# Performance work log

Hardware: AMD Instinct MI355X
Metric: run time of the kernel (lower is better)

## Reference

```python
import jax, jax.numpy as jnp
import numpy as np

HEADS = 8
DIM_HEAD = 64
SCALE = 10.0
EPS = 1e-12  # F.normalize eps


def setup_inputs() -> dict:
    key = jax.random.key(0)
    k1, k2, k3, k4 = jax.random.split(key, 4)
    dim, hidden = 256, HEADS * DIM_HEAD
    x = jax.random.normal(k1, (8, dim, 32, 32), dtype=jnp.float32)
    w_qkv = jax.random.normal(k2, (3 * hidden, dim), dtype=jnp.float32) * (1.0 / np.sqrt(dim))
    w_out = jax.random.normal(k3, (dim, hidden), dtype=jnp.float32) * (1.0 / np.sqrt(hidden))
    b_out = jax.random.normal(k4, (dim,), dtype=jnp.float32) * 0.01
    return {"x": x, "w_qkv": w_qkv, "w_out": w_out, "b_out": b_out}


def _l2norm_last(t):
    # matches F.normalize(t, dim=-1): t / max(||t||_2, eps)
    n = jnp.sqrt(jnp.sum(t * t, axis=-1, keepdims=True))
    return t / jnp.maximum(n, EPS)


def reference(x, w_qkv, w_out, b_out):
    b, c, hh, ww = x.shape
    n = hh * ww
    # 1x1 conv == channel matmul
    qkv = jnp.einsum('bcxy,oc->boxy', x, w_qkv)  # (b, 3*hidden, h, w)
    q, k, v = jnp.split(qkv, 3, axis=1)
    # 'b (h c) x y -> b h c (x y)'
    to_heads = lambda t: t.reshape(b, HEADS, DIM_HEAD, n)
    q, k, v = to_heads(q), to_heads(k), to_heads(v)
    # NOTE: l2norm over the LAST axis = spatial token axis n (faithful to source)
    q = _l2norm_last(q)
    k = _l2norm_last(k)
    sim = jnp.einsum('bhdi,bhdj->bhij', q, k) * SCALE  # (b, h, n, n)
    attn = jax.nn.softmax(sim, axis=-1)
    out = jnp.einsum('bhij,bhdj->bhid', attn, v)  # (b, h, n, d)
    # 'b h (x y) d -> b (h d) x y'
    out = out.transpose(0, 1, 3, 2).reshape(b, HEADS * DIM_HEAD, hh, ww)
    return jnp.einsum('bcxy,oc->boxy', out, w_out) + b_out[None, :, None, None]
```

## Files before the change

### kernel.cpp

```cpp
#include <hip/hip_runtime.h>
#include <math.h>

#define NHEADS 8
#define DHEAD  64
#define HIDDEN 512
#define CIN    256
#define NTOK   1024
#define QK_SCALE 10.0f
#define LOG2E 1.44269504088896f
#define MSHIFT 10.5f
#define MBIAS  (-MSHIFT * LOG2E)

typedef __bf16 bf16x8 __attribute__((ext_vector_type(8)));
typedef float  f32x4  __attribute__((ext_vector_type(4)));
typedef unsigned u32x4 __attribute__((ext_vector_type(4)));
typedef unsigned short u16x8 __attribute__((ext_vector_type(8)));
typedef unsigned short u16x4 __attribute__((ext_vector_type(4)));

__device__ inline unsigned short f2bf(float f) {
    unsigned u = __builtin_bit_cast(unsigned, f);
    u = (u + 0x7FFFu + ((u >> 16) & 1u)) >> 16;
    return (unsigned short)u;
}

__device__ inline unsigned pk2(float a, float b) {
    return (unsigned)f2bf(a) | ((unsigned)f2bf(b) << 16);
}

__device__ inline float bf2f(unsigned short u) {
    return __builtin_bit_cast(float, (unsigned)u << 16);
}

__device__ inline bf16x8 cvt8(const float* p) {
    float4 a = *(const float4*)p;
    float4 b = *(const float4*)(p + 4);
    u16x8 t;
    t[0] = f2bf(a.x); t[1] = f2bf(a.y); t[2] = f2bf(a.z); t[3] = f2bf(a.w);
    t[4] = f2bf(b.x); t[5] = f2bf(b.y); t[6] = f2bf(b.z); t[7] = f2bf(b.w);
    return __builtin_bit_cast(bf16x8, t);
}

__global__ __launch_bounds__(256)
void cvt_x_kernel(const float* __restrict__ x, unsigned short* __restrict__ xt) {
    const int b  = blockIdx.z;
    const int c0 = blockIdx.y * 64;
    const int n0 = blockIdx.x * 64;
    const float* src = x + ((size_t)b * CIN + c0) * NTOK + n0;
    unsigned short* dst = xt + ((size_t)b * NTOK + n0) * CIN + c0;

    __shared__ float T[64][65];
    const int t = threadIdx.x;
    {
        const int nq = t & 15, cg = t >> 4;
        #pragma unroll
        for (int rr = 0; rr < 4; ++rr) {
            const int c = cg + rr * 16;
            float4 v = *(const float4*)(src + (size_t)c * NTOK + nq * 4);
            T[c][nq * 4 + 0] = v.x;
            T[c][nq * 4 + 1] = v.y;
            T[c][nq * 4 + 2] = v.z;
            T[c][nq * 4 + 3] = v.w;
        }
    }
    __syncthreads();
    {
        const int n = t >> 2, cq = t & 3;
        alignas(16) unsigned short tmp[16];
        #pragma unroll
        for (int e = 0; e < 16; ++e)
            tmp[e] = f2bf(T[cq * 16 + e][n]);
        *(uint4*)(dst + (size_t)n * CIN + cq * 16)     = *(uint4*)&tmp[0];
        *(uint4*)(dst + (size_t)n * CIN + cq * 16 + 8) = *(uint4*)&tmp[8];
    }
}

__global__ __launch_bounds__(256)
void cvt_w_kernel(const float* __restrict__ wq, const float* __restrict__ wo,
                  unsigned short* __restrict__ wqb, unsigned short* __restrict__ wob) {
    const size_t i = ((size_t)blockIdx.x * 256 + threadIdx.x) * 8;
    if (i < (size_t)1536 * 256) {
        *(bf16x8*)(wqb + i) = cvt8(wq + i);
    } else {
        const size_t j = i - (size_t)1536 * 256;
        *(bf16x8*)(wob + j) = cvt8(wo + j);
    }
}

__global__ __launch_bounds__(256)
void gemm1_kernel(const unsigned short* __restrict__ wqb,
                  const unsigned short* __restrict__ xt,
                  float* __restrict__ qt,
                  unsigned short* __restrict__ vb,
                  float* __restrict__ ss) {
    const int b  = blockIdx.z;
    const int bm = blockIdx.y * 128;
    const int bn = blockIdx.x * 128;
    const int wave = threadIdx.x >> 6, lane = threadIdx.x & 63;
    const int lo = lane & 15, hi = lane >> 4;
    const int wm = bm + (wave >> 1) * 64;
    const int wn = bn + (wave & 1) * 64;

    const unsigned short* Ab = wqb + (size_t)(wm + lo) * CIN + hi * 8;
    const unsigned short* Bb = xt + ((size_t)b * NTOK + wn + lo) * CIN + hi * 8;

    f32x4 acc[4][4];
    #pragma unroll
    for (int mi = 0; mi < 4; ++mi)
        #pragma unroll
        for (int ni = 0; ni < 4; ++ni) acc[mi][ni] = (f32x4){0.f, 0.f, 0.f, 0.f};

    for (int k0 = 0; k0 < CIN; k0 += 32) {
        bf16x8 a[4], bf[4];
        #pragma unroll
        for (int mi = 0; mi < 4; ++mi) a[mi]  = *(const bf16x8*)(Ab + (size_t)mi * 16 * CIN + k0);
        #pragma unroll
        for (int ni = 0; ni < 4; ++ni) bf[ni] = *(const bf16x8*)(Bb + (size_t)ni * 16 * CIN + k0);
        #pragma unroll
        for (int mi = 0; mi < 4; ++mi)
            #pragma unroll
            for (int ni = 0; ni < 4; ++ni)
                acc[mi][ni] = __builtin_amdgcn_mfma_f32_16x16x32_bf16(a[mi], bf[ni], acc[mi][ni], 0, 0, 0);
    }

    __shared__ unsigned short VL[4][32][72];

    if (bm < 1024) {
        const int isK = (wm >= 512) ? 1 : 0;
        const int ch0 = wm & 511;
        const int head = ch0 >> 6;
        float* dst = qt + (((size_t)isK * 64 + b * 8 + head) * NTOK) * DHEAD;
        #pragma unroll
        for (int mi = 0; mi < 4; ++mi) {
            const int d = mi * 16 + hi * 4;
            #pragma unroll
            for (int ni = 0; ni < 4; ++ni) {
                const int n = wn + ni * 16 + lo;
                *(f32x4*)(dst + (size_t)n * DHEAD + d) = acc[mi][ni];
            }
        }
        float p[4][4];
        #pragma unroll
        for (int mi = 0; mi < 4; ++mi)
            #pragma unroll
            for (int r = 0; r < 4; ++r) {
                float s = 0.f;
                #pragma unroll
                for (int ni = 0; ni < 4; ++ni) s += acc[mi][ni][r] * acc[mi][ni][r];
                p[mi][r] = s;
            }
        #pragma unroll
        for (int off = 1; off < 16; off <<= 1)
            #pragma unroll
            for (int mi = 0; mi < 4; ++mi)
                #pragma unroll
                for (int r = 0; r < 4; ++r)
                    p[mi][r] += __shfl_xor(p[mi][r], off, 64);
        if (lo == 0) {
            #pragma unroll
            for (int mi = 0; mi < 4; ++mi)
                #pragma unroll
                for (int r = 0; r < 4; ++r)
                    atomicAdd(&ss[(size_t)b * 1024 + isK * 512 + ch0 + mi * 16 + hi * 4 + r], p[mi][r]);
        }
    } else {
        const int ch0 = wm - 1024;
        #pragma unroll
        for (int half = 0; half < 2; ++half) {
            #pragma unroll
            for (int mm = 0; mm < 2; ++mm) {
                const int mi = half * 2 + mm;
                #pragma unroll
                for (int ni = 0; ni < 4; ++ni)
                    #pragma unroll
                    for (int r = 0; r < 4; ++r)
                        VL[wave][mm * 16 + hi * 4 + r][ni * 16 + lo] = f2bf(acc[mi][ni][r]);
            }
            #pragma unroll
            for (int i = 0; i < 4; ++i) {
                const int flat = i * 64 + lane;
                const int row = flat >> 3, c = flat & 7;
                const int tb = c >> 2, hg = c & 3;
                const uint2 vlo = *(uint2*)&VL[wave][row][tb * 32 + hg * 4];
                const uint2 vhi = *(uint2*)&VL[wave][row][tb * 32 + hg * 4 + 16];
                uint4 v = make_uint4(vlo.x, vlo.y, vhi.x, vhi.y);
                const int ch = ch0 + half * 32 + row;
                *(uint4*)(vb + ((size_t)b * HIDDEN + ch) * NTOK + wn + c * 8) = v;
            }
        }
    }
}

__global__ __launch_bounds__(256)
void scale_cvt_kernel(const float* __restrict__ qt, const float* __restrict__ ss,
                      unsigned short* __restrict__ qs, unsigned short* __restrict__ ks) {
    const size_t idx = ((size_t)blockIdx.x * 256 + threadIdx.x) * 8;
    const size_t half = (size_t)64 * NTOK * DHEAD;
    const int isK = idx >= half;
    const size_t rem = idx - (size_t)isK * half;
    const int bh = (int)(rem >> 16);
    const int d0 = (int)(rem & 63);
    const int b  = bh >> 3;
    const int ch = isK * 512 + (bh & 7) * 64 + d0;
    const float scl = isK ? 1.0f : QK_SCALE;

    const float* ip = qt + idx;
    float4 v0 = *(const float4*)ip;
    float4 v1 = *(const float4*)(ip + 4);
    float4 q0 = *(const float4*)(ss + (size_t)b * 1024 + ch);
    float4 q1 = *(const float4*)(ss + (size_t)b * 1024 + ch + 4);
    float4 s0, s1;
    s0.x = 1.0f / fmaxf(sqrtf(q0.x), 1e-12f); s0.y = 1.0f / fmaxf(sqrtf(q0.y), 1e-12f);
    s0.z = 1.0f / fmaxf(sqrtf(q0.z), 1e-12f); s0.w = 1.0f / fmaxf(sqrtf(q0.w), 1e-12f);
    s1.x = 1.0f / fmaxf(sqrtf(q1.x), 1e-12f); s1.y = 1.0f / fmaxf(sqrtf(q1.y), 1e-12f);
    s1.z = 1.0f / fmaxf(sqrtf(q1.z), 1e-12f); s1.w = 1.0f / fmaxf(sqrtf(q1.w), 1e-12f);
    u16x8 t;
    t[0] = f2bf(v0.x * s0.x * scl); t[1] = f2bf(v0.y * s0.y * scl);
    t[2] = f2bf(v0.z * s0.z * scl); t[3] = f2bf(v0.w * s0.w * scl);
    t[4] = f2bf(v1.x * s1.x * scl); t[5] = f2bf(v1.y * s1.y * scl);
    t[6] = f2bf(v1.z * s1.z * scl); t[7] = f2bf(v1.w * s1.w * scl);
    *(u16x8*)((isK ? ks : qs) + rem) = t;
}

__global__ __launch_bounds__(128)
void attn_mfma_kernel(const unsigned short* __restrict__ qs,
                      const unsigned short* __restrict__ ks,
                      const unsigned short* __restrict__ vb,
                      unsigned short* __restrict__ po, float* __restrict__ pml) {
    const int hw = blockIdx.x;
    const int virt = (hw & 7) * 256 + (hw >> 3);
    const int bh  = virt >> 5;
    const int sub = virt & 31;
    const int it  = sub & 15;
    const int js  = sub >> 4;
    const int b = bh >> 3, h = bh & 7;

    const int lane = threadIdx.x & 63;
    const int wave = threadIdx.x >> 6;
    const int lo = lane & 15;
    const int hi = lane >> 4;
    const int iw = it * 64 + wave * 32;

    const unsigned short* qbh = qs + (size_t)bh * NTOK * DHEAD;
    const unsigned short* kbh = ks + (size_t)bh * NTOK * DHEAD;
    const unsigned short* vbh = vb + ((size_t)b * HIDDEN + h * DHEAD) * NTOK;

    bf16x8 aQ[2][2];
    #pragma unroll
    for (int f = 0; f < 2; ++f) {
        const unsigned short* qp = qbh + (size_t)(iw + f * 16 + lo) * DHEAD + hi * 8;
        aQ[f][0] = *(const bf16x8*)qp;
        aQ[f][1] = *(const bf16x8*)(qp + 32);
    }

    float lsum4[2][4];
    #pragma unroll
    for (int f = 0; f < 2; ++f)
        #pragma unroll
        for (int r = 0; r < 4; ++r) lsum4[f][r] = 0.0f;
    f32x4 acc[2][4];
    #pragma unroll
    for (int f = 0; f < 2; ++f)
        #pragma unroll
        for (int ds = 0; ds < 4; ++ds) acc[f][ds] = (f32x4){0.f, 0.f, 0.f, 0.f};

    for (int jt = 0; jt < 8; ++jt) {
        const int j0 = js * 512 + jt * 64;

        bf16x8 bV[4][2];
        #pragma unroll
        for (int ds = 0; ds < 4; ++ds) {
            const unsigned short* vp = vbh + (size_t)(ds * 16 + lo) * NTOK + j0 + hi * 8;
            bV[ds][0] = *(const bf16x8*)vp;
            bV[ds][1] = *(const bf16x8*)(vp + 32);
        }

        bf16x8 bK[4][2];
        #pragma unroll
        for (int jj = 0; jj < 4; ++jj) {
            const unsigned short* kp = kbh + (size_t)(j0 + jj * 16 + lo) * DHEAD + hi * 8;
            bK[jj][0] = *(const bf16x8*)kp;
            bK[jj][1] = *(const bf16x8*)(kp + 32);
        }

        f32x4 s[2][4];
        __builtin_amdgcn_s_setprio(1);
        #pragma unroll
        for (int jj = 0; jj < 4; ++jj)
            #pragma unroll
            for (int f = 0; f < 2; ++f) {
                f32x4 c = (f32x4){0.f, 0.f, 0.f, 0.f};
                c = __builtin_amdgcn_mfma_f32_16x16x32_bf16(bK[jj][0], aQ[f][0], c, 0, 0, 0);
                c = __builtin_amdgcn_mfma_f32_16x16x32_bf16(bK[jj][1], aQ[f][1], c, 0, 0, 0);
                s[f][jj] = c;
            }
        __builtin_amdgcn_s_setprio(0);

        unsigned pw[2][2][4];
        #pragma unroll
        for (int f = 0; f < 2; ++f) {
            #pragma unroll
            for (int jj = 0; jj < 4; ++jj)
                #pragma unroll
                for (int r = 0; r < 4; ++r) {
                    const float p = __builtin_amdgcn_exp2f(fmaf(s[f][jj][r], LOG2E, MBIAS));
                    s[f][jj][r] = p;
                    lsum4[f][r] += p;
                }
            #pragma unroll
            for (int t = 0; t < 2; ++t) {
                pw[f][t][0] = pk2(s[f][2 * t][0],     s[f][2 * t][1]);
                pw[f][t][1] = pk2(s[f][2 * t][2],     s[f][2 * t][3]);
                pw[f][t][2] = pk2(s[f][2 * t + 1][0], s[f][2 * t + 1][1]);
                pw[f][t][3] = pk2(s[f][2 * t + 1][2], s[f][2 * t + 1][3]);
            }
        }

        __builtin_amdgcn_s_setprio(1);
        #pragma unroll
        for (int ds = 0; ds < 4; ++ds)
            #pragma unroll
            for (int f = 0; f < 2; ++f)
                #pragma unroll
                for (int t = 0; t < 2; ++t) {
                    const bf16x8 bp = __builtin_bit_cast(bf16x8,
                        (u32x4){pw[f][t][0], pw[f][t][1], pw[f][t][2], pw[f][t][3]});
                    acc[f][ds] = __builtin_amdgcn_mfma_f32_16x16x32_bf16(bV[ds][t], bp, acc[f][ds], 0, 0, 0);
                }
        __builtin_amdgcn_s_setprio(0);
    }

    float lsum[2];
    #pragma unroll
    for (int f = 0; f < 2; ++f) {
        lsum[f] = (lsum4[f][0] + lsum4[f][1]) + (lsum4[f][2] + lsum4[f][3]);
        lsum[f] += __shfl_xor(lsum[f], 16, 64);
        lsum[f] += __shfl_xor(lsum[f], 32, 64);
    }

    unsigned short* pob = po + ((size_t)(js * 64 + bh) * NTOK + iw) * DHEAD;
    #pragma unroll
    for (int f = 0; f < 2; ++f) {
        #pragma unroll
        for (int ds = 0; ds < 4; ++ds) {
            uint2 w;
            w.x = pk2(acc[f][ds][0], acc[f][ds][1]);
            w.y = pk2(acc[f][ds][2], acc[f][ds][3]);
            *(uint2*)(pob + (size_t)(f * 16 + lo) * DHEAD + ds * 16 + hi * 4) = w;
        }
        if (hi == 0)
            pml[(size_t)(js * 64 + bh) * NTOK + iw + f * 16 + lo] = lsum[f];
    }
}

__global__ __launch_bounds__(256)
void combine_kernel(const unsigned short* __restrict__ po, const float* __restrict__ pml,
                    unsigned short* __restrict__ attn_t) {
    const size_t fl = ((size_t)blockIdx.x * 256 + threadIdx.x) * 4;
    const int bh  = (int)(fl >> 16);
    const int rem = (int)(fl & 65535);
    const int row = rem >> 6;
    const int d   = rem & 63;
    const int b = bh >> 3, h = bh & 7;
    const size_t SS = (size_t)64 * NTOK * DHEAD;

    const float l1 = pml[(size_t)bh * NTOK + row];
    const float l2 = pml[(size_t)(64 + bh) * NTOK + row];
    const float inv = 1.0f / (l1 + l2);

    const u16x4 o1 = *(const u16x4*)(po + fl);
    const u16x4 o2 = *(const u16x4*)(po + SS + fl);
    u16x4 r;
    #pragma unroll
    for (int e = 0; e < 4; ++e)
        r[e] = f2bf((bf2f(o1[e]) + bf2f(o2[e])) * inv);
    *(u16x4*)(attn_t + ((size_t)b * NTOK + row) * HIDDEN + h * DHEAD + d) = r;
}

__global__ __launch_bounds__(128)
void gemm2_kernel(const unsigned short* __restrict__ wob,
                  const unsigned short* __restrict__ attn_t,
                  const float* __restrict__ b_out,
                  float* __restrict__ out) {
    const int b  = blockIdx.z;
    const int bm = blockIdx.y * 64;
    const int bn = blockIdx.x * 128;
    const int wave = threadIdx.x >> 6, lane = threadIdx.x & 63;
    const int lo = lane & 15, hi = lane >> 4;
    const int wn = bn + wave * 64;

    const unsigned short* Ab = wob + (size_t)(bm + lo) * HIDDEN + hi * 8;
    const unsigned short* Bb = attn_t + ((size_t)b * NTOK + wn + lo) * HIDDEN + hi * 8;

    f32x4 acc[4][4];
    #pragma unroll
    for (int mi = 0; mi < 4; ++mi)
        #pragma unroll
        for (int ni = 0; ni < 4; ++ni) acc[mi][ni] = (f32x4){0.f, 0.f, 0.f, 0.f};

    for (int k0 = 0; k0 < HIDDEN; k0 += 32) {
        bf16x8 a[4], bf[4];
        #pragma unroll
        for (int mi = 0; mi < 4; ++mi) a[mi]  = *(const bf16x8*)(Ab + (size_t)mi * 16 * HIDDEN + k0);
        #pragma unroll
        for (int ni = 0; ni < 4; ++ni) bf[ni] = *(const bf16x8*)(Bb + (size_t)ni * 16 * HIDDEN + k0);
        #pragma unroll
        for (int mi = 0; mi < 4; ++mi)
            #pragma unroll
            for (int ni = 0; ni < 4; ++ni)
                acc[mi][ni] = __builtin_amdgcn_mfma_f32_16x16x32_bf16(a[mi], bf[ni], acc[mi][ni], 0, 0, 0);
    }

    __shared__ float OL[2][32][69];
    #pragma unroll
    for (int half = 0; half < 2; ++half) {
        #pragma unroll
        for (int mm = 0; mm < 2; ++mm) {
            const int mi = half * 2 + mm;
            #pragma unroll
            for (int ni = 0; ni < 4; ++ni)
                #pragma unroll
                for (int r = 0; r < 4; ++r)
                    OL[wave][mm * 16 + hi * 4 + r][ni * 16 + lo] = acc[mi][ni][r];
        }
        #pragma unroll
        for (int i = 0; i < 8; ++i) {
            const int flat = i * 64 + lane;
            const int row = flat >> 4, c = flat & 15;
            float4 v = *(float4*)&OL[wave][row][c * 4];
            const int m = bm + half * 32 + row;
            const float bb = b_out[m];
            v.x += bb; v.y += bb; v.z += bb; v.w += bb;
            *(float4*)(out + ((size_t)b * CIN + m) * NTOK + wn + c * 4) = v;
        }
    }
}

extern "C" void kernel_launch(void* const* d_in, const int* in_sizes, int n_in,
                              void* d_out, int out_size, void* d_ws, size_t ws_size,
                              hipStream_t stream) {
    const float* x     = (const float*)d_in[0];
    const float* w_qkv = (const float*)d_in[1];
    const float* w_out = (const float*)d_in[2];
    const float* b_out = (const float*)d_in[3];
    float* out = (float*)d_out;

    char* ws = (char*)d_ws;
    unsigned short* xt  = (unsigned short*)(ws);
    unsigned short* wqb = (unsigned short*)(ws + 4194304);
    unsigned short* wob = (unsigned short*)(ws + 4980736);
    float*          ss  = (float*)(ws + 5242880);
    unsigned short* qs  = (unsigned short*)(ws + 5308416);
    unsigned short* ks  = (unsigned short*)(ws + 13697024);
    unsigned short* vb  = (unsigned short*)(ws + 22085632);
    float*          qt  = (float*)(ws + 30474240);
    unsigned short* po  = (unsigned short*)(ws + 30474240);
    unsigned short* attn_t = (unsigned short*)(ws + 5308416);
    float*          pml = (float*)(ws + 64028672);

    hipMemsetAsync(ss, 0, 8 * 1024 * sizeof(float), stream);

    cvt_x_kernel<<<dim3(16, 4, 8), 256, 0, stream>>>(x, xt);
    cvt_w_kernel<<<256, 256, 0, stream>>>(w_qkv, w_out, wqb, wob);

    gemm1_kernel<<<dim3(8, 12, 8), 256, 0, stream>>>(wqb, xt, qt, vb, ss);

    scale_cvt_kernel<<<4096, 256, 0, stream>>>(qt, ss, qs, ks);

    attn_mfma_kernel<<<2048, 128, 0, stream>>>(qs, ks, vb, po, pml);

    combine_kernel<<<4096, 256, 0, stream>>>(po, pml, attn_t);

    gemm2_kernel<<<dim3(8, 4, 8), 128, 0, stream>>>(wob, attn_t, b_out, out);
}
```

Before: 203.5 us.

## Split attention keys four ways and pack probabilities by bf16 truncation

The attention kernel now splits each query tile's keys across four partitions instead of two. This doubles the block count to 4096, halves the per-block loop, and unrolls it by two, aiming at better occupancy and latency hiding. Probability packing switches from round-to-nearest to bit truncation, and the row sums accumulate the truncated values so numerator and denominator stay consistent. The combine kernel sums four partials and processes eight elements per thread, but now reads twice as much partial-output data from memory, and the larger po/pml buffers depend on the workspace being big enough.

```diff
diff --git a/kernel.cpp b/kernel.cpp
--- a/kernel.cpp
+++ b/kernel.cpp
@@ -10,6 +10,7 @@
 #define LOG2E 1.44269504088896f
 #define MSHIFT 10.5f
 #define MBIAS  (-MSHIFT * LOG2E)
+#define NSPLIT 4
 
 typedef __bf16 bf16x8 __attribute__((ext_vector_type(8)));
 typedef float  f32x4  __attribute__((ext_vector_type(4)));
@@ -25,6 +26,14 @@
 
 __device__ inline unsigned pk2(float a, float b) {
     return (unsigned)f2bf(a) | ((unsigned)f2bf(b) << 16);
+}
+
+__device__ inline unsigned pk2t(float a, float b) {
+    return (__builtin_bit_cast(unsigned, a) >> 16) |
+           (__builtin_bit_cast(unsigned, b) & 0xFFFF0000u);
+}
+__device__ inline float trunc_bf(float f) {
+    return __builtin_bit_cast(float, __builtin_bit_cast(unsigned, f) & 0xFFFF0000u);
 }
 
 __device__ inline float bf2f(unsigned short u) {
@@ -227,9 +236,9 @@
                       const unsigned short* __restrict__ vb,
                       unsigned short* __restrict__ po, float* __restrict__ pml) {
     const int hw = blockIdx.x;
-    const int virt = (hw & 7) * 256 + (hw >> 3);
-    const int bh  = virt >> 5;
-    const int sub = virt & 31;
+    const int virt = (hw & 7) * 512 + (hw >> 3);
+    const int bh  = virt >> 6;
+    const int sub = virt & 63;
     const int it  = sub & 15;
     const int js  = sub >> 4;
     const int b = bh >> 3, h = bh & 7;
@@ -263,8 +272,9 @@
         #pragma unroll
         for (int ds = 0; ds < 4; ++ds) acc[f][ds] = (f32x4){0.f, 0.f, 0.f, 0.f};
 
-    for (int jt = 0; jt < 8; ++jt) {
-        const int j0 = js * 512 + jt * 64;
+    #pragma unroll 2
+    for (int jt = 0; jt < 4; ++jt) {
+        const int j0 = js * 256 + jt * 64;
 
         bf16x8 bV[4][2];
         #pragma unroll
@@ -304,14 +314,14 @@
                 for (int r = 0; r < 4; ++r) {
                     const float p = __builtin_amdgcn_exp2f(fmaf(s[f][jj][r], LOG2E, MBIAS));
                     s[f][jj][r] = p;
-                    lsum4[f][r] += p;
+                    lsum4[f][r] += trunc_bf(p);
                 }
             #pragma unroll
             for (int t = 0; t < 2; ++t) {
-                pw[f][t][0] = pk2(s[f][2 * t][0],     s[f][2 * t][1]);
-                pw[f][t][1] = pk2(s[f][2 * t][2],     s[f][2 * t][3]);
-                pw[f][t][2] = pk2(s[f][2 * t + 1][0], s[f][2 * t + 1][1]);
-                pw[f][t][3] = pk2(s[f][2 * t + 1][2], s[f][2 * t + 1][3]);
+                pw[f][t][0] = pk2t(s[f][2 * t][0],     s[f][2 * t][1]);
+                pw[f][t][1] = pk2t(s[f][2 * t][2],     s[f][2 * t][3]);
+                pw[f][t][2] = pk2t(s[f][2 * t + 1][0], s[f][2 * t + 1][1]);
+                pw[f][t][3] = pk2t(s[f][2 * t + 1][2], s[f][2 * t + 1][3]);
             }
         }
 
@@ -355,7 +365,7 @@
 __global__ __launch_bounds__(256)
 void combine_kernel(const unsigned short* __restrict__ po, const float* __restrict__ pml,
                     unsigned short* __restrict__ attn_t) {
-    const size_t fl = ((size_t)blockIdx.x * 256 + threadIdx.x) * 4;
+    const size_t fl = ((size_t)blockIdx.x * 256 + threadIdx.x) * 8;
     const int bh  = (int)(fl >> 16);
     const int rem = (int)(fl & 65535);
     const int row = rem >> 6;
@@ -363,17 +373,23 @@
     const int b = bh >> 3, h = bh & 7;
     const size_t SS = (size_t)64 * NTOK * DHEAD;
 
-    const float l1 = pml[(size_t)bh * NTOK + row];
-    const float l2 = pml[(size_t)(64 + bh) * NTOK + row];
-    const float inv = 1.0f / (l1 + l2);
-
-    const u16x4 o1 = *(const u16x4*)(po + fl);
-    const u16x4 o2 = *(const u16x4*)(po + SS + fl);
-    u16x4 r;
-    #pragma unroll
-    for (int e = 0; e < 4; ++e)
-        r[e] = f2bf((bf2f(o1[e]) + bf2f(o2[e])) * inv);
-    *(u16x4*)(attn_t + ((size_t)b * NTOK + row) * HIDDEN + h * DHEAD + d) = r;
+    float l = 0.f;
+    #pragma unroll
+    for (int s = 0; s < NSPLIT; ++s)
+        l += pml[(size_t)(s * 64 + bh) * NTOK + row];
+    const float inv = 1.0f / l;
+
+    float o[8] = {};
+    #pragma unroll
+    for (int s = 0; s < NSPLIT; ++s) {
+        const u16x8 v = *(const u16x8*)(po + s * SS + fl);
+        #pragma unroll
+        for (int e = 0; e < 8; ++e) o[e] += bf2f(v[e]);
+    }
+    u16x8 r;
+    #pragma unroll
+    for (int e = 0; e < 8; ++e) r[e] = f2bf(o[e] * inv);
+    *(u16x8*)(attn_t + ((size_t)b * NTOK + row) * HIDDEN + h * DHEAD + d) = r;
 }
 
 __global__ __launch_bounds__(128)
@@ -466,9 +482,9 @@
 
     scale_cvt_kernel<<<4096, 256, 0, stream>>>(qt, ss, qs, ks);
 
-    attn_mfma_kernel<<<2048, 128, 0, stream>>>(qs, ks, vb, po, pml);
-
-    combine_kernel<<<4096, 256, 0, stream>>>(po, pml, attn_t);
+    attn_mfma_kernel<<<4096, 128, 0, stream>>>(qs, ks, vb, po, pml);
+
+    combine_kernel<<<2048, 256, 0, stream>>>(po, pml, attn_t);
 
     gemm2_kernel<<<dim3(8, 4, 8), 128, 0, stream>>>(wob, attn_t, b_out, out);
 }
```

After: 207.8 us. +2.1%, slower.
